# Kernel tuning notes

Measured on AMD Instinct MI355X. Metric: run time of the kernel, lower is better.

Reference implementation:

```python
import jax, jax.numpy as jnp
import numpy as np

SMOOTH = 1e-06
LAMBDA_FOCAL = 1.0
LAMBDA_DICE = 1.0
LAMBDA_BOUNDARY = 0.5
LAMBDA_CONTRASTIVE = 0.1
ALPHA = 0.25
GAMMA = 2.0
NUM_IDS = 32  # instance ids in [0, NUM_IDS); 0 = background


def _sobel_grad(x):
    """Kornia-style normalized sobel spatial gradient with replicate padding.
    x: [B,1,H,W] -> (gx, gy) each [B,1,H,W]."""
    kx = jnp.array([[-1., 0., 1.], [-2., 0., 2.], [-1., 0., 1.]], x.dtype) / 8.0  # abs-sum normalized
    ky = kx.T
    k = jnp.stack([kx, ky])[:, None]  # [2,1,3,3]
    xp = jnp.pad(x, ((0, 0), (0, 0), (1, 1), (1, 1)), mode='edge')
    out = jax.lax.conv_general_dilated(xp, k, (1, 1), 'VALID',
                                       dimension_numbers=('NCHW', 'OIHW', 'NCHW'))
    return out[:, 0:1], out[:, 1:2]


def _forward(predictions, targets, instance_masks):
    p = jnp.clip(jax.nn.sigmoid(predictions), SMOOTH, 1.0 - SMOOTH)  # [B,H,W]
    t = jnp.clip(targets, 0.0, 1.0)

    # ---- focal loss ----
    bce = -(t * jnp.log(p) + (1.0 - t) * jnp.log1p(-p))
    pt = jnp.where(t == 1.0, p, 1.0 - p)
    focal_w = (1.0 - pt) ** GAMMA
    alpha_w = jnp.where(t == 1.0, ALPHA, 1.0 - ALPHA)
    focal = jnp.mean(alpha_w * focal_w * bce)

    # ---- dice loss ----
    inter = jnp.sum(p * t)
    dice = 1.0 - (2.0 * inter + SMOOTH) / (jnp.sum(p) + jnp.sum(t) + SMOOTH)

    # ---- boundary loss (sobel gradient magnitude + direction) ----
    p4, t4 = p[:, None], t[:, None]  # [B,1,H,W]
    tgx, tgy = _sobel_grad(t4)
    pgx, pgy = _sobel_grad(p4)
    tmag = jnp.sqrt(tgx ** 2 + tgy ** 2 + 1e-6)
    pmag = jnp.sqrt(pgx ** 2 + pgy ** 2 + 1e-6)
    bw = 1.0 + 5.0 * tmag
    loss_mag = jnp.mean((pmag * bw - tmag * bw) ** 2)
    mask = (tmag > 0.1).astype(p.dtype)
    cos = (tgx / tmag) * (pgx / pmag) + (tgy / tmag) * (pgy / pmag)
    msum = jnp.sum(mask)
    dir_loss = jnp.where(msum > 0, jnp.sum((1.0 - cos) * mask) / jnp.maximum(msum, 1.0), 0.0)
    boundary = loss_mag + dir_loss

    # ---- instance contrastive loss (segment-mean + pairwise exp distance) ----
    B = p.shape[0]
    ids = instance_masks.reshape(B, -1).astype(jnp.int32)
    flat_ids = (ids + jnp.arange(B, dtype=jnp.int32)[:, None] * NUM_IDS).reshape(-1)
    pf = p.reshape(-1)
    sums = jax.ops.segment_sum(pf, flat_ids, num_segments=B * NUM_IDS).reshape(B, NUM_IDS)
    cnts = jax.ops.segment_sum(jnp.ones_like(pf), flat_ids, num_segments=B * NUM_IDS).reshape(B, NUM_IDS)
    means = sums / jnp.maximum(cnts, 1.0)  # [B,K]
    ks = jnp.arange(NUM_IDS)
    valid = (cnts > 0) & (ks[None, :] > 0)  # exclude background id 0
    diff = jnp.abs(means[:, :, None] - means[:, None, :])  # [B,K,K]
    pair = (valid[:, :, None] & valid[:, None, :] & (ks[:, None] < ks[None, :])).astype(p.dtype)
    npairs = jnp.sum(pair, axis=(1, 2))
    csum = jnp.sum(jnp.exp(-diff) * pair, axis=(1, 2))
    contrastive = jnp.sum(jnp.where(npairs > 0, csum / jnp.maximum(npairs, 1.0), 0.0)) / B

    return (LAMBDA_FOCAL * focal + LAMBDA_DICE * dice
            + LAMBDA_BOUNDARY * boundary + LAMBDA_CONTRASTIVE * contrastive)


def setup_inputs() -> dict:
    key = jax.random.key(0)
    k1, k2, k3 = jax.random.split(key, 3)
    B, H, W = 16, 1024, 1024
    predictions = jax.random.normal(k1, (B, H, W), dtype=jnp.float32)
    targets = jnp.round(jax.random.uniform(k2, (B, H, W), dtype=jnp.float32))  # binary masks
    instance_masks = jax.random.randint(k3, (B, H, W), 0, NUM_IDS, dtype=jnp.int32)
    return {"predictions": predictions, "targets": targets, "instance_masks": instance_masks}


def reference(predictions, targets, instance_masks):
    return _forward(predictions, targets, instance_masks)
```

## Files before the change

### kernel.cpp

```cpp
#include <hip/hip_runtime.h>
#include <math.h>

#define HH 1024
#define WW 1024
#define BB 16
#define RR 8
#define NID 32
#define NPX (1ull * BB * HH * WW)
#define CBIT 41
#define SSCALE 262144.0f
#define INV_SSCALE 3.814697265625e-06f


__device__ __forceinline__ float fast_rcp(float x) {
  float r; asm("v_rcp_f32 %0, %1" : "=v"(r) : "v"(x)); return r;
}
__device__ __forceinline__ float fast_rsq(float x) {
  float r; asm("v_rsq_f32 %0, %1" : "=v"(r) : "v"(x)); return r;
}
__device__ __forceinline__ float sigc(float x) {
  float p = fast_rcp(1.f + __expf(-x));
  return fminf(fmaxf(p, 1e-6f), 1.f - 1e-6f);
}

__global__ __launch_bounds__(256, 3) void seg_main(
    const float* __restrict__ pred, const float* __restrict__ targ,
    const int* __restrict__ ids, float* __restrict__ acc,
    unsigned long long* __restrict__ seg_pack) {
  __shared__ unsigned long long s_pack[NID];
  __shared__ float red[4][8];

  const int tid = threadIdx.x;
  const int b  = blockIdx.x >> 7;
  const int rg = blockIdx.x & 127;
  const int h0 = rg * RR;
  const int w0 = tid * 4;
  const int wl = (w0 == 0) ? 0 : w0 - 1;
  const int wr = (w0 == WW - 4) ? WW - 1 : w0 + 4;

  if (tid < NID) s_pack[tid] = 0ull;
  __syncthreads();

  const size_t base = (size_t)b * HH * WW;
  const float*  pb  = pred + base;
  const float*  tb  = targ + base;
  const float4* pb4 = (const float4*)pb;
  const float4* tb4 = (const float4*)tb;
  const int4*   ib4 = (const int4*)(ids + base);

  float facc = 0.f, iacc = 0.f, pacc = 0.f, macc = 0.f, dacc = 0.f;
  int   tcnt = 0, kcnt = 0;

  float Pa0, Pa1, Pa2, Pa3, Pa4, Pa5;
  float Pb0, Pb1, Pb2, Pb3, Pb4, Pb5;
  float Pc0, Pc1, Pc2, Pc3, Pc4, Pc5;
  int   Ma, Mb, Mc;
  float4 nx, nt;
  float nxl, nxr, ntl, ntr;
  int4 IDa, IDb;

#define LOADRAW(h)                                                     \
  do { int hh = (h); hh = hh < 0 ? 0 : (hh > HH - 1 ? HH - 1 : hh);    \
    nx  = pb4[hh * (WW / 4) + tid];                                    \
    nxl = pb[hh * WW + wl];  nxr = pb[hh * WW + wr];                   \
    nt  = tb4[hh * (WW / 4) + tid];                                    \
    ntl = tb[hh * WW + wl];  ntr = tb[hh * WW + wr];                   \
  } while (0)

#define SIG(P, M)                                                      \
  do {                                                                 \
    P##0 = sigc(nxl);  P##1 = sigc(nx.x); P##2 = sigc(nx.y);           \
    P##3 = sigc(nx.z); P##4 = sigc(nx.w); P##5 = sigc(nxr);            \
    M = (ntl  >= 0.5f ? 1  : 0) | (nt.x >= 0.5f ? 2  : 0)              \
      | (nt.y >= 0.5f ? 4  : 0) | (nt.z >= 0.5f ? 8  : 0)              \
      | (nt.w >= 0.5f ? 16 : 0) | (ntr  >= 0.5f ? 32 : 0);             \
  } while (0)

#define PIX(PA, PB, PC, MA, MB, MC, c0, c1, c2, idj)                   \
  do {                                                                 \
    float p = PB##c1;                                                  \
    const int one = (MB >> (c1)) & 1;                                  \
    float pt = one ? p : 1.f - p;                                      \
    float om = 1.f - pt;                                               \
    facc += (one ? 0.25f : 0.75f) * om * om * (-__logf(pt));           \
    iacc += one ? p : 0.f;                                             \
    pacc += p;                                                         \
    tcnt += one;                                                       \
    int a0 = (MA >> (c0)) & 1, a1 = (MA >> (c1)) & 1,                  \
        a2 = (MA >> (c2)) & 1;                                         \
    int b0 = (MB >> (c0)) & 1, b2 = (MB >> (c2)) & 1;                  \
    int d0 = (MC >> (c0)) & 1, d1 = (MC >> (c1)) & 1,                  \
        d2 = (MC >> (c2)) & 1;                                         \
    int gxi = (a2 - a0) + 2 * (b2 - b0) + (d2 - d0);                   \
    int gyi = (d0 - a0) + 2 * (d1 - a1) + (d2 - a2);                   \
    float tgx = (float)gxi * 0.125f;                                   \
    float tgy = (float)gyi * 0.125f;                                   \
    float m2t = tgx * tgx + tgy * tgy + 1e-6f;                         \
    float rst = fast_rsq(m2t);                                         \
    float tmag = m2t * rst;                                            \
    float pgx = (PA##c2 - PA##c0 + 2.f * (PB##c2 - PB##c0)             \
               + PC##c2 - PC##c0) * 0.125f;                            \
    float pgy = (PC##c0 - PA##c0 + 2.f * (PC##c1 - PA##c1)             \
               + PC##c2 - PA##c2) * 0.125f;                            \
    float m2p = pgx * pgx + pgy * pgy + 1e-6f;                         \
    float rsp = fast_rsq(m2p);                                         \
    float pmag = m2p * rsp;                                            \
    float bwv = 1.f + 5.f * tmag;                                      \
    float d = (pmag - tmag) * bwv;                                     \
    macc += d * d;                                                     \
    if ((gxi | gyi) != 0) {                                            \
      dacc += 1.f - (tgx * pgx + tgy * pgy) * (rst * rsp);             \
      kcnt += 1;                                                       \
    }                                                                  \
    unsigned int q = __float2uint_rn(p * SSCALE);                      \
    atomicAdd(&s_pack[idj], (1ull << CBIT) | (unsigned long long)q);   \
  } while (0)

#define BODY(PA, PB, PC, MA, MB, MC, IDU, IDN, r)                      \
  do {                                                                 \
    SIG(PC, MC);                                                       \
    if ((r) < RR - 1) {                                                \
      LOADRAW(h0 + (r) + 2);                                           \
      IDN = ib4[(h0 + (r) + 1) * (WW / 4) + tid];                      \
    }                                                                  \
    PIX(PA, PB, PC, MA, MB, MC, 0, 1, 2, IDU.x);                       \
    PIX(PA, PB, PC, MA, MB, MC, 1, 2, 3, IDU.y);                       \
    PIX(PA, PB, PC, MA, MB, MC, 2, 3, 4, IDU.z);                       \
    PIX(PA, PB, PC, MA, MB, MC, 3, 4, 5, IDU.w);                       \
    __builtin_amdgcn_sched_barrier(0);                                 \
  } while (0)

  LOADRAW(h0 - 1); SIG(Pa, Ma);
  LOADRAW(h0);     SIG(Pb, Mb);
  LOADRAW(h0 + 1);
  IDa = ib4[h0 * (WW / 4) + tid];
  __builtin_amdgcn_sched_barrier(0);

  BODY(Pa, Pb, Pc, Ma, Mb, Mc, IDa, IDb, 0);
  BODY(Pb, Pc, Pa, Mb, Mc, Ma, IDb, IDa, 1);
  BODY(Pc, Pa, Pb, Mc, Ma, Mb, IDa, IDb, 2);
  BODY(Pa, Pb, Pc, Ma, Mb, Mc, IDb, IDa, 3);
  BODY(Pb, Pc, Pa, Mb, Mc, Ma, IDa, IDb, 4);
  BODY(Pc, Pa, Pb, Mc, Ma, Mb, IDb, IDa, 5);
  BODY(Pa, Pb, Pc, Ma, Mb, Mc, IDa, IDb, 6);
  BODY(Pb, Pc, Pa, Mb, Mc, Ma, IDb, IDa, 7);

#undef LOADRAW
#undef SIG
#undef PIX
#undef BODY

  float tacc = (float)tcnt;
  float kacc = (float)kcnt;
#define WRED(x)                                                        \
  do { _Pragma("unroll")                                               \
    for (int off = 32; off > 0; off >>= 1) x += __shfl_down(x, off, 64); \
  } while (0)
  WRED(facc); WRED(iacc); WRED(pacc); WRED(tacc);
  WRED(macc); WRED(dacc); WRED(kacc);
#undef WRED
  int wave = tid >> 6, lane = tid & 63;
  if (lane == 0) {
    red[wave][0] = facc; red[wave][1] = iacc; red[wave][2] = pacc;
    red[wave][3] = tacc; red[wave][4] = macc; red[wave][5] = dacc;
    red[wave][6] = kacc;
  }
  __syncthreads();
  if (tid < 7) {
    atomicAdd(&acc[tid], red[0][tid] + red[1][tid] + red[2][tid] + red[3][tid]);
  }
  if (tid < NID) {
    atomicAdd(&seg_pack[b * NID + tid], s_pack[tid]);
  }
}

__global__ void seg_final(const float* __restrict__ acc,
                          const unsigned long long* __restrict__ seg_pack,
                          float* __restrict__ out) {
  __shared__ float contr[BB];
  int tid = threadIdx.x;
  int b   = tid >> 4;
  int l16 = tid & 15;
  if (b < BB) {
    float means[NID];
    bool  val[NID];
    #pragma unroll
    for (int k = 0; k < NID; ++k) {
      unsigned long long v = seg_pack[b * NID + k];
      float cnt = (float)(v >> CBIT);
      float sum = (float)(v & ((1ull << CBIT) - 1)) * INV_SSCALE;
      means[k] = sum / fmaxf(cnt, 1.f);
      val[k] = (cnt > 0.f) && (k > 0);
    }
    float csum = 0.f, np = 0.f;
    int cnt = 0;
    #pragma unroll
    for (int k = 0; k < NID; ++k) {
      #pragma unroll
      for (int l = k + 1; l < NID; ++l) {
        if ((cnt & 15) == l16) {
          if (val[k] && val[l]) {
            csum += __expf(-fabsf(means[k] - means[l]));
            np += 1.f;
          }
        }
        ++cnt;
      }
    }
    #pragma unroll
    for (int off = 1; off < 16; off <<= 1) {
      csum += __shfl_xor(csum, off, 16);
      np   += __shfl_xor(np,   off, 16);
    }
    if (l16 == 0) contr[b] = (np > 0.f) ? csum / fmaxf(np, 1.f) : 0.f;
  }
  __syncthreads();
  if (tid == 0) {
    float c = 0.f;
    for (int b2 = 0; b2 < BB; ++b2) c += contr[b2];
    c /= (float)BB;
    float N = (float)NPX;
    float focal = acc[0] / N;
    float dice  = 1.f - (2.f * acc[1] + 1e-6f) / (acc[2] + acc[3] + 1e-6f);
    float dir   = (acc[6] > 0.f) ? acc[5] / fmaxf(acc[6], 1.f) : 0.f;
    float boundary = acc[4] / N + dir;
    out[0] = focal + dice + 0.5f * boundary + 0.1f * c;
  }
}

extern "C" void kernel_launch(void* const* d_in, const int* in_sizes, int n_in,
                              void* d_out, int out_size, void* d_ws, size_t ws_size,
                              hipStream_t stream) {
  const float* pred = (const float*)d_in[0];
  const float* targ = (const float*)d_in[1];
  const int*   ids  = (const int*)d_in[2];
  float* acc = (float*)d_ws;
  unsigned long long* seg_pack = (unsigned long long*)((char*)d_ws + 64);

  hipMemsetAsync(d_ws, 0, 64 + BB * NID * sizeof(unsigned long long), stream);

  int blocks = BB * (HH / RR);
  seg_main<<<blocks, 256, 0, stream>>>(pred, targ, ids, acc, seg_pack);
  seg_final<<<1, 256, 0, stream>>>(acc, seg_pack, (float*)d_out);
}
```

Baseline: 71.66 us.

## Share halo columns via wave shuffles, pack instance ids, halve rows per block

```diff
diff --git a/kernel.cpp b/kernel.cpp
--- a/kernel.cpp
+++ b/kernel.cpp
@@ -4,7 +4,7 @@
 #define HH 1024
 #define WW 1024
 #define BB 16
-#define RR 8
+#define RR 4
 #define NID 32
 #define NPX (1ull * BB * HH * WW)
 #define CBIT 41
@@ -19,8 +19,7 @@
   float r; asm("v_rsq_f32 %0, %1" : "=v"(r) : "v"(x)); return r;
 }
 __device__ __forceinline__ float sigc(float x) {
-  float p = fast_rcp(1.f + __expf(-x));
-  return fminf(fmaxf(p, 1e-6f), 1.f - 1e-6f);
+  return fast_rcp(1.f + __expf(-x));
 }
 
 __global__ __launch_bounds__(256, 3) void seg_main(
@@ -31,12 +30,17 @@
   __shared__ float red[4][8];
 
   const int tid = threadIdx.x;
-  const int b  = blockIdx.x >> 7;
-  const int rg = blockIdx.x & 127;
+  const int b  = blockIdx.x >> 8;
+  const int rg = blockIdx.x & 255;
   const int h0 = rg * RR;
   const int w0 = tid * 4;
   const int wl = (w0 == 0) ? 0 : w0 - 1;
   const int wr = (w0 == WW - 4) ? WW - 1 : w0 + 4;
+  const int lane = tid & 63;
+  const bool edge0  = (lane == 0);
+  const bool edge63 = (lane == 63);
+  const bool edge   = edge0 || edge63;
+  const int  we     = edge0 ? wl : wr;
 
   if (tid < NID) s_pack[tid] = 0ull;
   __syncthreads();
@@ -56,27 +60,41 @@
   float Pc0, Pc1, Pc2, Pc3, Pc4, Pc5;
   int   Ma, Mb, Mc;
   float4 nx, nt;
-  float nxl, nxr, ntl, ntr;
-  int4 IDa, IDb;
+  float xe = 0.f, te = 0.f;
+  unsigned int IDa, IDb;
 
 #define LOADRAW(h)                                                     \
   do { int hh = (h); hh = hh < 0 ? 0 : (hh > HH - 1 ? HH - 1 : hh);    \
-    nx  = pb4[hh * (WW / 4) + tid];                                    \
-    nxl = pb[hh * WW + wl];  nxr = pb[hh * WW + wr];                   \
-    nt  = tb4[hh * (WW / 4) + tid];                                    \
-    ntl = tb[hh * WW + wl];  ntr = tb[hh * WW + wr];                   \
-  } while (0)
-
-#define SIG(P, M)                                                      \
+    nx = pb4[hh * (WW / 4) + tid];                                     \
+    nt = tb4[hh * (WW / 4) + tid];                                     \
+    if (edge) { xe = pb[hh * WW + we]; te = tb[hh * WW + we]; }        \
+  } while (0)
+
+#define LOADID(h) (( (unsigned int)ib4[(h) * (WW / 4) + tid].x        ) | \
+                   ( (unsigned int)ib4[(h) * (WW / 4) + tid].y << 8   ) | \
+                   ( (unsigned int)ib4[(h) * (WW / 4) + tid].z << 16  ) | \
+                   ( (unsigned int)ib4[(h) * (WW / 4) + tid].w << 24  ))
+
+#define SIGS(P, M)                                                     \
   do {                                                                 \
-    P##0 = sigc(nxl);  P##1 = sigc(nx.x); P##2 = sigc(nx.y);           \
-    P##3 = sigc(nx.z); P##4 = sigc(nx.w); P##5 = sigc(nxr);            \
-    M = (ntl  >= 0.5f ? 1  : 0) | (nt.x >= 0.5f ? 2  : 0)              \
-      | (nt.y >= 0.5f ? 4  : 0) | (nt.z >= 0.5f ? 8  : 0)              \
-      | (nt.w >= 0.5f ? 16 : 0) | (ntr  >= 0.5f ? 32 : 0);             \
-  } while (0)
-
-#define PIX(PA, PB, PC, MA, MB, MC, c0, c1, c2, idj)                   \
+    P##1 = sigc(nx.x); P##2 = sigc(nx.y);                              \
+    P##3 = sigc(nx.z); P##4 = sigc(nx.w);                              \
+    float Pe = sigc(xe);                                               \
+    int m4 = (nt.x >= 0.5f ? 1 : 0) | (nt.y >= 0.5f ? 2 : 0)           \
+           | (nt.z >= 0.5f ? 4 : 0) | (nt.w >= 0.5f ? 8 : 0);          \
+    int me4 = (te >= 0.5f) ? 15 : 0;                                   \
+    float Pl = __shfl_up(P##4, 1, 64);                                 \
+    float Pr = __shfl_down(P##1, 1, 64);                               \
+    int  msl = __shfl_up(m4, 1, 64);                                   \
+    int  msr = __shfl_down(m4, 1, 64);                                 \
+    P##0 = edge0  ? Pe : Pl;                                           \
+    P##5 = edge63 ? Pe : Pr;                                           \
+    int mlb = ((edge0  ? me4 : msl) >> 3) & 1;                         \
+    int mrb =  (edge63 ? me4 : msr) & 1;                               \
+    M = (m4 << 1) | mlb | (mrb << 5);                                  \
+  } while (0)
+
+#define PIX(PA, PB, PC, MA, MB, MC, c0, c1, c2, sh, IDU)               \
   do {                                                                 \
     float p = PB##c1;                                                  \
     const int one = (MB >> (c1)) & 1;                                  \
@@ -112,41 +130,39 @@
       dacc += 1.f - (tgx * pgx + tgy * pgy) * (rst * rsp);             \
       kcnt += 1;                                                       \
     }                                                                  \
+    unsigned int idj = ((IDU) >> (sh)) & 31u;                          \
     unsigned int q = __float2uint_rn(p * SSCALE);                      \
     atomicAdd(&s_pack[idj], (1ull << CBIT) | (unsigned long long)q);   \
   } while (0)
 
 #define BODY(PA, PB, PC, MA, MB, MC, IDU, IDN, r)                      \
   do {                                                                 \
-    SIG(PC, MC);                                                       \
+    SIGS(PC, MC);                                                      \
     if ((r) < RR - 1) {                                                \
       LOADRAW(h0 + (r) + 2);                                           \
-      IDN = ib4[(h0 + (r) + 1) * (WW / 4) + tid];                      \
+      IDN = LOADID(h0 + (r) + 1);                                      \
     }                                                                  \
-    PIX(PA, PB, PC, MA, MB, MC, 0, 1, 2, IDU.x);                       \
-    PIX(PA, PB, PC, MA, MB, MC, 1, 2, 3, IDU.y);                       \
-    PIX(PA, PB, PC, MA, MB, MC, 2, 3, 4, IDU.z);                       \
-    PIX(PA, PB, PC, MA, MB, MC, 3, 4, 5, IDU.w);                       \
+    PIX(PA, PB, PC, MA, MB, MC, 0, 1, 2, 0,  IDU);                     \
+    PIX(PA, PB, PC, MA, MB, MC, 1, 2, 3, 8,  IDU);                     \
+    PIX(PA, PB, PC, MA, MB, MC, 2, 3, 4, 16, IDU);                     \
+    PIX(PA, PB, PC, MA, MB, MC, 3, 4, 5, 24, IDU);                     \
     __builtin_amdgcn_sched_barrier(0);                                 \
   } while (0)
 
-  LOADRAW(h0 - 1); SIG(Pa, Ma);
-  LOADRAW(h0);     SIG(Pb, Mb);
+  LOADRAW(h0 - 1); SIGS(Pa, Ma);
+  LOADRAW(h0);     SIGS(Pb, Mb);
   LOADRAW(h0 + 1);
-  IDa = ib4[h0 * (WW / 4) + tid];
+  IDa = LOADID(h0);
   __builtin_amdgcn_sched_barrier(0);
 
   BODY(Pa, Pb, Pc, Ma, Mb, Mc, IDa, IDb, 0);
   BODY(Pb, Pc, Pa, Mb, Mc, Ma, IDb, IDa, 1);
   BODY(Pc, Pa, Pb, Mc, Ma, Mb, IDa, IDb, 2);
   BODY(Pa, Pb, Pc, Ma, Mb, Mc, IDb, IDa, 3);
-  BODY(Pb, Pc, Pa, Mb, Mc, Ma, IDa, IDb, 4);
-  BODY(Pc, Pa, Pb, Mc, Ma, Mb, IDb, IDa, 5);
-  BODY(Pa, Pb, Pc, Ma, Mb, Mc, IDa, IDb, 6);
-  BODY(Pb, Pc, Pa, Mb, Mc, Ma, IDb, IDa, 7);
 
 #undef LOADRAW
-#undef SIG
+#undef LOADID
+#undef SIGS
 #undef PIX
 #undef BODY
 
@@ -159,8 +175,8 @@
   WRED(facc); WRED(iacc); WRED(pacc); WRED(tacc);
   WRED(macc); WRED(dacc); WRED(kacc);
 #undef WRED
-  int wave = tid >> 6, lane = tid & 63;
-  if (lane == 0) {
+  int wave = tid >> 6, lane2 = tid & 63;
+  if (lane2 == 0) {
     red[wave][0] = facc; red[wave][1] = iacc; red[wave][2] = pacc;
     red[wave][3] = tacc; red[wave][4] = macc; red[wave][5] = dacc;
     red[wave][6] = kacc;
```

Result: slower. 91.58 us (+27.8%).
